# Kernel optimization log

Hardware: AMD Instinct MI355X
Metric: run time of the kernel (lower is better)

The kernel has to match this reference:

```python
import jax, jax.numpy as jnp
import numpy as np

N_NODES = 50000
N_EDGES = 800000
NUM_FEATURES = 128
HIDDEN = 128
EMBED = 64
OUT_DIM = 1


def setup_inputs() -> dict:
    key = jax.random.key(0)
    ks = jax.random.split(key, 12)
    x = jax.random.normal(ks[0], (N_NODES, NUM_FEATURES), dtype=jnp.float32)
    edge_index = jax.random.randint(ks[1], (2, N_EDGES), 0, N_NODES, dtype=jnp.int64)

    def glorot(k, fan_in, fan_out):
        s = jnp.sqrt(6.0 / (fan_in + fan_out)).astype(jnp.float32)
        return jax.random.uniform(k, (fan_in, fan_out), jnp.float32, -s, s)

    return {
        "x": x,
        "edge_index": edge_index,
        "W1": glorot(ks[2], NUM_FEATURES, HIDDEN),
        "b1": jnp.zeros((HIDDEN,), jnp.float32),
        "Wh": glorot(ks[3], HIDDEN, HIDDEN),
        "bh": jnp.zeros((HIDDEN,), jnp.float32),
        "W2": glorot(ks[4], HIDDEN, EMBED),
        "b2": jnp.zeros((EMBED,), jnp.float32),
        "Wout": glorot(ks[5], EMBED, OUT_DIM),
        "bout": jnp.zeros((OUT_DIM,), jnp.float32),
    }


def _gcn_norm(edge_index, num_nodes):
    # Add self-loops, compute symmetric normalization deg^{-1/2} A_hat deg^{-1/2}
    loop = jnp.arange(num_nodes, dtype=edge_index.dtype)
    src = jnp.concatenate([edge_index[0], loop])
    dst = jnp.concatenate([edge_index[1], loop])
    deg = jax.ops.segment_sum(jnp.ones_like(dst, dtype=jnp.float32), dst,
                              num_segments=num_nodes)
    dis = jnp.where(deg > 0, jax.lax.rsqrt(jnp.maximum(deg, 1.0)), 0.0)
    norm = dis[src] * dis[dst]  # [E+N]
    return src, dst, norm


def _gcn_conv(h, W, b, src, dst, norm, num_nodes):
    h = h @ W  # linear transform first (PyG GCNConv)
    msg = h[src] * norm[:, None]  # gather + scale
    return jax.ops.segment_sum(msg, dst, num_segments=num_nodes) + b


def reference(x, edge_index, W1, b1, Wh, bh, W2, b2, Wout, bout):
    n = x.shape[0]
    src, dst, norm = _gcn_norm(edge_index, n)
    h = jax.nn.relu(_gcn_conv(x, W1, b1, src, dst, norm, n))  # dropout p=0 -> identity
    h = jax.nn.relu(_gcn_conv(h, Wh, bh, src, dst, norm, n))
    h = _gcn_conv(h, W2, b2, src, dst, norm, n)
    out = h @ Wout + bout
    return (out, h)
```

## Files before the change

kernel.cpp:

```cpp
#include <hip/hip_runtime.h>
#include <hip/hip_bf16.h>


#define N_NODES 50000
#define N_EDGES 800000
#define NBUCK 196
#define GB 196
#define EPB 4096

typedef __attribute__((ext_vector_type(8))) short short8;
typedef __attribute__((ext_vector_type(8))) unsigned short ushort8v;
typedef __attribute__((ext_vector_type(4))) float f32x4;

static __device__ __forceinline__ unsigned short f2bf(float f) {
    __hip_bfloat16 h = __float2bfloat16(f);
    return *reinterpret_cast<unsigned short*>(&h);
}
static __device__ __forceinline__ float bf2f(unsigned short u) {
    return __uint_as_float(((unsigned)u) << 16);
}


__global__ __launch_bounds__(256) void hist_wprep_kernel(
    const int* __restrict__ dstv, int* __restrict__ H, int nE, int* __restrict__ ticket,
    const float* __restrict__ W1, const float* __restrict__ Wh, const float* __restrict__ W2,
    unsigned short* __restrict__ W1hi, unsigned short* __restrict__ W1lo,
    unsigned short* __restrict__ Whhi, unsigned short* __restrict__ Whlo,
    unsigned short* __restrict__ W2hi, unsigned short* __restrict__ W2lo) {
    int gt = blockIdx.x * 256 + threadIdx.x;
    if (gt == 0) *ticket = 0;
    if (gt < 40960) {
        const float* W;
        unsigned short *Hi, *Lo;
        int nout, lt;
        if (gt < 16384)      { W = W1; Hi = W1hi; Lo = W1lo; nout = 128; lt = gt; }
        else if (gt < 32768) { W = Wh; Hi = Whhi; Lo = Whlo; nout = 128; lt = gt - 16384; }
        else                 { W = W2; Hi = W2hi; Lo = W2lo; nout = 64;  lt = gt - 32768; }
        int col = lt % nout, k = lt / nout;
        float v = W[lt];
        unsigned short hi = f2bf(v);
        unsigned short lo = f2bf(v - bf2f(hi));
        Hi[(size_t)col * 128 + k] = hi;
        Lo[(size_t)col * 128 + k] = lo;
    }

    __shared__ int h[NBUCK];
    for (int i = threadIdx.x; i < NBUCK; i += 256) h[i] = 0;
    __syncthreads();
    int base = blockIdx.x * EPB;
#pragma unroll
    for (int i = 0; i < EPB / 256; ++i) {
        int e = base + i * 256 + threadIdx.x;
        if (e < nE) atomicAdd(&h[dstv[e] >> 8], 1);
    }
    __syncthreads();
    for (int i = threadIdx.x; i < NBUCK; i += 256)
        H[i * GB + blockIdx.x] = h[i];
}

__global__ __launch_bounds__(256) void scan_kernel(int* __restrict__ H,
                                                   int* __restrict__ bsum,
                                                   int* __restrict__ bstart,
                                                   int* __restrict__ rowoff_last,
                                                   int* __restrict__ ticket) {
    __shared__ int s[256];
    __shared__ int lastFlag;
    int t = threadIdx.x;
    int k = blockIdx.x;
    int v = (t < GB) ? H[k * GB + t] : 0;
    s[t] = v;
    __syncthreads();
    for (int off = 1; off < 256; off <<= 1) {
        int u = (t >= off) ? s[t - off] : 0;
        __syncthreads();
        s[t] += u;
        __syncthreads();
    }
    if (t < GB) H[k * GB + t] = s[t] - v;
    if (t == 255) {
        bsum[k] = s[255];
        __threadfence();
        int tk = atomicAdd(ticket, 1);
        lastFlag = (tk == NBUCK - 1);
    }
    __syncthreads();
    if (!lastFlag) return;
    __threadfence();
    int v2 = (t < NBUCK) ? bsum[t] : 0;
    s[t] = v2;
    __syncthreads();
    for (int off = 1; off < 256; off <<= 1) {
        int u = (t >= off) ? s[t - off] : 0;
        __syncthreads();
        s[t] += u;
        __syncthreads();
    }
    if (t < NBUCK) bstart[t] = s[t] - v2;
    if (t == 0) {
        bstart[NBUCK] = N_EDGES;
        *rowoff_last = N_EDGES;
    }
}

__global__ __launch_bounds__(256) void partition_kernel(const int* __restrict__ srcv,
                                                        const int* __restrict__ dstv,
                                                        const int* __restrict__ H,
                                                        const int* __restrict__ bstart,
                                                        unsigned int* __restrict__ P, int nE) {
    __shared__ int cur[NBUCK];
    for (int i = threadIdx.x; i < NBUCK; i += 256)
        cur[i] = bstart[i] + H[i * GB + blockIdx.x];
    __syncthreads();
    int base = blockIdx.x * EPB;
#pragma unroll
    for (int i = 0; i < EPB / 256; ++i) {
        int e = base + i * 256 + threadIdx.x;
        if (e < nE) {
            int d = dstv[e];
            unsigned int pk = (unsigned int)srcv[e] | ((unsigned int)(d & 255) << 16);
            int pos = atomicAdd(&cur[d >> 8], 1);
            P[pos] = pk;
        }
    }
}

__global__ __launch_bounds__(256) void bucket_csr_kernel(const unsigned int* __restrict__ P,
                                                         const int* __restrict__ bstart,
                                                         int* __restrict__ rowoff,
                                                         float* __restrict__ dis,
                                                         unsigned short* __restrict__ csr_src, int n) {
    __shared__ int cnt[256];
    __shared__ int s[256];
    __shared__ int cur[256];
    int t = threadIdx.x;
    int k = blockIdx.x;
    int ebeg = bstart[k], eend = bstart[k + 1];
    cnt[t] = 0;
    __syncthreads();
    for (int e = ebeg + t; e < eend; e += 256)
        atomicAdd(&cnt[(P[e] >> 16) & 255], 1);
    __syncthreads();
    int myc = cnt[t];
    s[t] = myc;
    __syncthreads();
    for (int off = 1; off < 256; off <<= 1) {
        int v = (t >= off) ? s[t - off] : 0;
        __syncthreads();
        s[t] += v;
        __syncthreads();
    }
    int excl = s[t] - myc;
    int node = (k << 8) + t;
    if (node < n) {
        rowoff[node] = ebeg + excl;
        dis[node] = rsqrtf((float)(myc + 1));
    }
    cur[t] = ebeg + excl;
    __syncthreads();
    for (int e = ebeg + t; e < eend; e += 256) {
        unsigned int p = P[e];
        int pos = atomicAdd(&cur[(p >> 16) & 255], 1);
        csr_src[pos] = (unsigned short)(p & 0xFFFFu);
    }
}

template <int NOUT, bool SPLITA>
__global__ __launch_bounds__(256) void gemm_mfma_kernel(
    const float* __restrict__ A,
    const unsigned short* __restrict__ Ahi,
    const unsigned short* __restrict__ Alo,
    const unsigned short* __restrict__ Wthi,
    const unsigned short* __restrict__ Wtlo,
    const float* __restrict__ scale,
    unsigned short* __restrict__ C, int M) {
    constexpr int LDK = 136;
    __shared__ unsigned short sAhi[64 * LDK];
    __shared__ unsigned short sAlo[64 * LDK];

    int tid = threadIdx.x;
    int w = tid >> 6, lane = tid & 63;
    int quad = lane >> 4, m = lane & 15;
    int Rbase = blockIdx.x * 64;
    int Cbase = blockIdx.y * 64;
    int r0 = (w & 1) * 32, c0 = (w >> 1) * 32;

    short8 bh[4][2], bl[4][2];
#pragma unroll
    for (int ks = 0; ks < 4; ++ks)
#pragma unroll
        for (int g = 0; g < 2; ++g) {
            size_t off = (size_t)(Cbase + c0 + g * 16 + m) * 128 + ks * 32 + quad * 8;
            bh[ks][g] = *(const short8*)(Wthi + off);
            bl[ks][g] = *(const short8*)(Wtlo + off);
        }

    if constexpr (SPLITA) {
        for (int i = tid; i < 64 * 16; i += 256) {
            int r = i >> 4, c8 = i & 15;
            int row = Rbase + r;
            short8 hv = {0, 0, 0, 0, 0, 0, 0, 0};
            short8 lv = {0, 0, 0, 0, 0, 0, 0, 0};
            if (row < M) {
                hv = *(const short8*)(Ahi + (size_t)row * 128 + c8 * 8);
                lv = *(const short8*)(Alo + (size_t)row * 128 + c8 * 8);
            }
            *(short8*)(sAhi + r * LDK + c8 * 8) = hv;
            *(short8*)(sAlo + r * LDK + c8 * 8) = lv;
        }
    } else {
        for (int i = tid; i < 64 * 32; i += 256) {
            int r = i >> 5, c4 = i & 31;
            int row = Rbase + r;
            float4 v = make_float4(0.f, 0.f, 0.f, 0.f);
            if (row < M) v = ((const float4*)(A + (size_t)row * 128))[c4];
            ushort4 hi, lo;
            hi.x = f2bf(v.x); lo.x = f2bf(v.x - bf2f(hi.x));
            hi.y = f2bf(v.y); lo.y = f2bf(v.y - bf2f(hi.y));
            hi.z = f2bf(v.z); lo.z = f2bf(v.z - bf2f(hi.z));
            hi.w = f2bf(v.w); lo.w = f2bf(v.w - bf2f(hi.w));
            *(ushort4*)(sAhi + r * LDK + c4 * 4) = hi;
            *(ushort4*)(sAlo + r * LDK + c4 * 4) = lo;
        }
    }
    __syncthreads();

    f32x4 z = {0.f, 0.f, 0.f, 0.f};
    f32x4 acc00 = z, acc01 = z, acc10 = z, acc11 = z;

#pragma unroll
    for (int ks = 0; ks < 4; ++ks) {
        int kof = ks * 32 + quad * 8;
        short8 ah0 = *(const short8*)(sAhi + (r0 + m) * LDK + kof);
        short8 ah1 = *(const short8*)(sAhi + (r0 + 16 + m) * LDK + kof);
        short8 al0 = *(const short8*)(sAlo + (r0 + m) * LDK + kof);
        short8 al1 = *(const short8*)(sAlo + (r0 + 16 + m) * LDK + kof);
        acc00 = __builtin_amdgcn_mfma_f32_16x16x32_bf16(ah0, bh[ks][0], acc00, 0, 0, 0);
        acc01 = __builtin_amdgcn_mfma_f32_16x16x32_bf16(ah0, bh[ks][1], acc01, 0, 0, 0);
        acc10 = __builtin_amdgcn_mfma_f32_16x16x32_bf16(ah1, bh[ks][0], acc10, 0, 0, 0);
        acc11 = __builtin_amdgcn_mfma_f32_16x16x32_bf16(ah1, bh[ks][1], acc11, 0, 0, 0);
        acc00 = __builtin_amdgcn_mfma_f32_16x16x32_bf16(ah0, bl[ks][0], acc00, 0, 0, 0);
        acc01 = __builtin_amdgcn_mfma_f32_16x16x32_bf16(ah0, bl[ks][1], acc01, 0, 0, 0);
        acc10 = __builtin_amdgcn_mfma_f32_16x16x32_bf16(ah1, bl[ks][0], acc10, 0, 0, 0);
        acc11 = __builtin_amdgcn_mfma_f32_16x16x32_bf16(ah1, bl[ks][1], acc11, 0, 0, 0);
        acc00 = __builtin_amdgcn_mfma_f32_16x16x32_bf16(al0, bh[ks][0], acc00, 0, 0, 0);
        acc01 = __builtin_amdgcn_mfma_f32_16x16x32_bf16(al0, bh[ks][1], acc01, 0, 0, 0);
        acc10 = __builtin_amdgcn_mfma_f32_16x16x32_bf16(al1, bh[ks][0], acc10, 0, 0, 0);
        acc11 = __builtin_amdgcn_mfma_f32_16x16x32_bf16(al1, bh[ks][1], acc11, 0, 0, 0);
    }

#pragma unroll
    for (int reg = 0; reg < 4; ++reg) {
        int row0g = Rbase + r0 + quad * 4 + reg;
        if (row0g < M) {
            float sc = scale[row0g];
            C[(size_t)row0g * NOUT + Cbase + c0 + m]      = f2bf(acc00[reg] * sc);
            C[(size_t)row0g * NOUT + Cbase + c0 + 16 + m] = f2bf(acc01[reg] * sc);
        }
        int row1g = row0g + 16;
        if (row1g < M) {
            float sc = scale[row1g];
            C[(size_t)row1g * NOUT + Cbase + c0 + m]      = f2bf(acc10[reg] * sc);
            C[(size_t)row1g * NOUT + Cbase + c0 + 16 + m] = f2bf(acc11[reg] * sc);
        }
    }
}

__global__ __launch_bounds__(256) void aggregate128_kernel(
    const int* __restrict__ rowoff, const unsigned short* __restrict__ csr_src,
    const float* __restrict__ dis, const unsigned short* __restrict__ tp,
    const float* __restrict__ bias,
    unsigned short* __restrict__ outHi, unsigned short* __restrict__ outLo, int n) {
    int wid = (blockIdx.x * 256 + threadIdx.x) >> 6;
    int lane = threadIdx.x & 63;
    int sub = lane >> 4, lc = lane & 15;
    int n0 = wid * 2;
    if (n0 >= n) return;
    int n1 = n0 + 1;
    bool has1 = (n1 < n);

    float a0[8] = {0.f, 0.f, 0.f, 0.f, 0.f, 0.f, 0.f, 0.f};
    float a1[8] = {0.f, 0.f, 0.f, 0.f, 0.f, 0.f, 0.f, 0.f};

#define ROW128(node) (*(const ushort8v*)(tp + (size_t)(node) * 128 + lc * 8))
#define ACC(a, u) { a[0] += bf2f(u[0]); a[1] += bf2f(u[1]); a[2] += bf2f(u[2]); a[3] += bf2f(u[3]); \
                    a[4] += bf2f(u[4]); a[5] += bf2f(u[5]); a[6] += bf2f(u[6]); a[7] += bf2f(u[7]); }

    if (sub == 0) { ushort8v u = ROW128(n0); ACC(a0, u); }
    else if (sub == 1 && has1) { ushort8v u = ROW128(n1); ACC(a1, u); }

    int mid = rowoff[n0 + 1];
    int i0 = rowoff[n0] + sub;
    int i1 = mid + sub;
    int end1 = has1 ? rowoff[n1 + 1] : mid;

    while (i0 + 12 < mid && i1 + 12 < end1) {
        int p0 = csr_src[i0], p1 = csr_src[i0 + 4], p2 = csr_src[i0 + 8], p3 = csr_src[i0 + 12];
        int q0 = csr_src[i1], q1 = csr_src[i1 + 4], q2 = csr_src[i1 + 8], q3 = csr_src[i1 + 12];
        ushort8v u0 = ROW128(p0), u1 = ROW128(p1), u2 = ROW128(p2), u3 = ROW128(p3);
        ushort8v v0 = ROW128(q0), v1 = ROW128(q1), v2 = ROW128(q2), v3 = ROW128(q3);
        ACC(a0, u0); ACC(a0, u1); ACC(a0, u2); ACC(a0, u3);
        ACC(a1, v0); ACC(a1, v1); ACC(a1, v2); ACC(a1, v3);
        i0 += 16; i1 += 16;
    }
    while (i0 + 4 < mid && i1 + 4 < end1) {
        int p0 = csr_src[i0], p1 = csr_src[i0 + 4];
        int q0 = csr_src[i1], q1 = csr_src[i1 + 4];
        ushort8v u0 = ROW128(p0), u1 = ROW128(p1);
        ushort8v v0 = ROW128(q0), v1 = ROW128(q1);
        ACC(a0, u0); ACC(a0, u1);
        ACC(a1, v0); ACC(a1, v1);
        i0 += 8; i1 += 8;
    }
    for (; i0 + 4 < mid; i0 += 8) {
        int p0 = csr_src[i0], p1 = csr_src[i0 + 4];
        ushort8v u0 = ROW128(p0), u1 = ROW128(p1);
        ACC(a0, u0); ACC(a0, u1);
    }
    for (; i0 < mid; i0 += 4) { ushort8v u = ROW128(csr_src[i0]); ACC(a0, u); }
    for (; i1 + 4 < end1; i1 += 8) {
        int q0 = csr_src[i1], q1 = csr_src[i1 + 4];
        ushort8v v0 = ROW128(q0), v1 = ROW128(q1);
        ACC(a1, v0); ACC(a1, v1);
    }
    for (; i1 < end1; i1 += 4) { ushort8v v = ROW128(csr_src[i1]); ACC(a1, v); }
#undef ROW128
#undef ACC

#pragma unroll
    for (int j = 0; j < 8; ++j) {
        a0[j] += __shfl_xor(a0[j], 16);
        a0[j] += __shfl_xor(a0[j], 32);
        a1[j] += __shfl_xor(a1[j], 16);
        a1[j] += __shfl_xor(a1[j], 32);
    }

    float* ap = (sub == 0) ? a0 : a1;
    int node = (sub == 0) ? n0 : n1;
    bool valid = (sub == 0) || (sub == 1 && has1);
    if (valid) {
        float dd = dis[node];
        float4 b0 = ((const float4*)bias)[lc * 2];
        float4 b1v = ((const float4*)bias)[lc * 2 + 1];
        float r[8];
        r[0] = fmaxf(ap[0] * dd + b0.x, 0.f);
        r[1] = fmaxf(ap[1] * dd + b0.y, 0.f);
        r[2] = fmaxf(ap[2] * dd + b0.z, 0.f);
        r[3] = fmaxf(ap[3] * dd + b0.w, 0.f);
        r[4] = fmaxf(ap[4] * dd + b1v.x, 0.f);
        r[5] = fmaxf(ap[5] * dd + b1v.y, 0.f);
        r[6] = fmaxf(ap[6] * dd + b1v.z, 0.f);
        r[7] = fmaxf(ap[7] * dd + b1v.w, 0.f);
        ushort8v hi, lo;
#pragma unroll
        for (int j = 0; j < 8; ++j) {
            hi[j] = f2bf(r[j]);
            lo[j] = f2bf(r[j] - bf2f(hi[j]));
        }
        *(ushort8v*)(outHi + (size_t)node * 128 + lc * 8) = hi;
        *(ushort8v*)(outLo + (size_t)node * 128 + lc * 8) = lo;
    }
}

__global__ __launch_bounds__(256) void aggregate64_head_kernel(
    const int* __restrict__ rowoff, const unsigned short* __restrict__ csr_src,
    const float* __restrict__ dis, const unsigned short* __restrict__ tp,
    const float* __restrict__ bias, const float* __restrict__ Wout,
    const float* __restrict__ bout, float* __restrict__ hout,
    float* __restrict__ out, int n) {
    int wid = (blockIdx.x * 256 + threadIdx.x) >> 6;
    int lane = threadIdx.x & 63;
    int sub = lane >> 4, lc = lane & 15;
    int n0 = wid * 2;
    if (n0 >= n) return;
    int n1 = n0 + 1;
    bool has1 = (n1 < n);

    float a0[4] = {0.f, 0.f, 0.f, 0.f};
    float a1[4] = {0.f, 0.f, 0.f, 0.f};

#define ROW64(node) (*((const ushort4*)(tp + (size_t)(node) * 64 + lc * 4)))
#define ACC2(a, u) { a[0] += bf2f(u.x); a[1] += bf2f(u.y); a[2] += bf2f(u.z); a[3] += bf2f(u.w); }

    if (sub == 0) { ushort4 u = ROW64(n0); ACC2(a0, u); }
    else if (sub == 1 && has1) { ushort4 u = ROW64(n1); ACC2(a1, u); }

    int mid = rowoff[n0 + 1];
    int i0 = rowoff[n0] + sub;
    int i1 = mid + sub;
    int end1 = has1 ? rowoff[n1 + 1] : mid;

    while (i0 + 12 < mid && i1 + 12 < end1) {
        int p0 = csr_src[i0], p1 = csr_src[i0 + 4], p2 = csr_src[i0 + 8], p3 = csr_src[i0 + 12];
        int q0 = csr_src[i1], q1 = csr_src[i1 + 4], q2 = csr_src[i1 + 8], q3 = csr_src[i1 + 12];
        ushort4 u0 = ROW64(p0), u1 = ROW64(p1), u2 = ROW64(p2), u3 = ROW64(p3);
        ushort4 v0 = ROW64(q0), v1 = ROW64(q1), v2 = ROW64(q2), v3 = ROW64(q3);
        ACC2(a0, u0); ACC2(a0, u1); ACC2(a0, u2); ACC2(a0, u3);
        ACC2(a1, v0); ACC2(a1, v1); ACC2(a1, v2); ACC2(a1, v3);
        i0 += 16; i1 += 16;
    }
    while (i0 + 4 < mid && i1 + 4 < end1) {
        int p0 = csr_src[i0], p1 = csr_src[i0 + 4];
        int q0 = csr_src[i1], q1 = csr_src[i1 + 4];
        ushort4 u0 = ROW64(p0), u1 = ROW64(p1);
        ushort4 v0 = ROW64(q0), v1 = ROW64(q1);
        ACC2(a0, u0); ACC2(a0, u1);
        ACC2(a1, v0); ACC2(a1, v1);
        i0 += 8; i1 += 8;
    }
    for (; i0 < mid; i0 += 4) { ushort4 u = ROW64(csr_src[i0]); ACC2(a0, u); }
    for (; i1 < end1; i1 += 4) { ushort4 v = ROW64(csr_src[i1]); ACC2(a1, v); }
#undef ROW64
#undef ACC2

#pragma unroll
    for (int j = 0; j < 4; ++j) {
        a0[j] += __shfl_xor(a0[j], 16);
        a0[j] += __shfl_xor(a0[j], 32);
        a1[j] += __shfl_xor(a1[j], 16);
        a1[j] += __shfl_xor(a1[j], 32);
    }

    float* ap = (sub == 0) ? a0 : a1;
    int node = (sub == 0) ? n0 : n1;
    bool valid = (sub == 0) || (sub == 1 && has1);
    float4 hv = make_float4(0.f, 0.f, 0.f, 0.f);
    if (valid) {
        float dd = dis[node];
        float4 b = ((const float4*)bias)[lc];
        hv.x = ap[0] * dd + b.x;
        hv.y = ap[1] * dd + b.y;
        hv.z = ap[2] * dd + b.z;
        hv.w = ap[3] * dd + b.w;
        ((float4*)(hout + (size_t)node * 64))[lc] = hv;
    }
    float4 wv = ((const float4*)Wout)[lc];
    float p = valid ? (hv.x * wv.x + hv.y * wv.y + hv.z * wv.z + hv.w * wv.w) : 0.f;
#pragma unroll
    for (int off = 8; off > 0; off >>= 1) p += __shfl_xor(p, off);
    if (lc == 0 && valid) out[node] = p + bout[0];
}

extern "C" void kernel_launch(void* const* d_in, const int* in_sizes, int n_in,
                              void* d_out, int out_size, void* d_ws, size_t ws_size,
                              hipStream_t stream) {
    const float* x    = (const float*)d_in[0];
    const int*   ei   = (const int*)d_in[1];
    const float* W1   = (const float*)d_in[2];
    const float* b1   = (const float*)d_in[3];
    const float* Wh   = (const float*)d_in[4];
    const float* bh   = (const float*)d_in[5];
    const float* W2   = (const float*)d_in[6];
    const float* b2   = (const float*)d_in[7];
    const float* Wout = (const float*)d_in[8];
    const float* bout = (const float*)d_in[9];

    const int N = N_NODES;
    const int E = N_EDGES;
    const int* srcv = ei;
    const int* dstv = ei + E;

    float* out  = (float*)d_out;
    float* hout = (float*)d_out + N;

    char* ws = (char*)d_ws;
    auto alloc = [&](size_t bytes) -> char* {
        char* p = ws;
        ws += (bytes + 255) & ~(size_t)255;
        return p;
    };
    int*   H       = (int*)alloc(sizeof(int) * NBUCK * GB);
    int*   bsum    = (int*)alloc(sizeof(int) * NBUCK);
    int*   bstart  = (int*)alloc(sizeof(int) * (NBUCK + 1));
    int*   ticket  = (int*)alloc(sizeof(int) * 4);
    int*   rowoff  = (int*)alloc(sizeof(int) * (N + 1));
    unsigned int* P = (unsigned int*)alloc(sizeof(unsigned int) * E);
    unsigned short* csr_src = (unsigned short*)alloc(sizeof(unsigned short) * (E + 2));
    float* dis     = (float*)alloc(sizeof(float) * N);
    unsigned short* W1thi = (unsigned short*)alloc(sizeof(unsigned short) * 128 * 128);
    unsigned short* W1tlo = (unsigned short*)alloc(sizeof(unsigned short) * 128 * 128);
    unsigned short* Whthi = (unsigned short*)alloc(sizeof(unsigned short) * 128 * 128);
    unsigned short* Whtlo = (unsigned short*)alloc(sizeof(unsigned short) * 128 * 128);
    unsigned short* W2thi = (unsigned short*)alloc(sizeof(unsigned short) * 64 * 128);
    unsigned short* W2tlo = (unsigned short*)alloc(sizeof(unsigned short) * 64 * 128);
    unsigned short* bufT  = (unsigned short*)alloc(sizeof(unsigned short) * (size_t)N * 128);
    unsigned short* bufHi = (unsigned short*)alloc(sizeof(unsigned short) * (size_t)N * 128);
    unsigned short* bufLo = (unsigned short*)alloc(sizeof(unsigned short) * (size_t)N * 128);

    hist_wprep_kernel<<<GB, 256, 0, stream>>>(dstv, H, E, ticket,
                                              W1, Wh, W2, W1thi, W1tlo, Whthi, Whtlo, W2thi, W2tlo);
    scan_kernel<<<NBUCK, 256, 0, stream>>>(H, bsum, bstart, rowoff + N, ticket);
    partition_kernel<<<GB, 256, 0, stream>>>(srcv, dstv, H, bstart, P, E);
    bucket_csr_kernel<<<NBUCK, 256, 0, stream>>>(P, bstart, rowoff, dis, csr_src, N);

    const int aggBlocks = ((N + 1) / 2 * 64 + 255) / 256;
    const int gemmRows = (N + 63) / 64;

    gemm_mfma_kernel<128, false><<<dim3(gemmRows, 2), 256, 0, stream>>>(
        x, nullptr, nullptr, W1thi, W1tlo, dis, bufT, N);
    aggregate128_kernel<<<aggBlocks, 256, 0, stream>>>(
        rowoff, csr_src, dis, bufT, b1, bufHi, bufLo, N);

    gemm_mfma_kernel<128, true><<<dim3(gemmRows, 2), 256, 0, stream>>>(
        nullptr, bufHi, bufLo, Whthi, Whtlo, dis, bufT, N);
    aggregate128_kernel<<<aggBlocks, 256, 0, stream>>>(
        rowoff, csr_src, dis, bufT, bh, bufHi, bufLo, N);

    gemm_mfma_kernel<64, true><<<dim3(gemmRows, 1), 256, 0, stream>>>(
        nullptr, bufHi, bufLo, W2thi, W2tlo, dis, bufT, N);
    aggregate64_head_kernel<<<aggBlocks, 256, 0, stream>>>(
        rowoff, csr_src, dis, bufT, b2, Wout, bout, hout, out, N);
}
```

Baseline: 277.9 us.

## Assign one 16-lane group per node in aggregation, dropping cross-lane reductions

```diff
diff --git a/kernel.cpp b/kernel.cpp
--- a/kernel.cpp
+++ b/kernel.cpp
@@ -19,7 +19,6 @@
 static __device__ __forceinline__ float bf2f(unsigned short u) {
     return __uint_as_float(((unsigned)u) << 16);
 }
-
 
 __global__ __launch_bounds__(256) void hist_wprep_kernel(
     const int* __restrict__ dstv, int* __restrict__ H, int nE, int* __restrict__ ticket,
@@ -30,9 +29,7 @@
     int gt = blockIdx.x * 256 + threadIdx.x;
     if (gt == 0) *ticket = 0;
     if (gt < 40960) {
-        const float* W;
-        unsigned short *Hi, *Lo;
-        int nout, lt;
+        const float* W; unsigned short *Hi, *Lo; int nout, lt;
         if (gt < 16384)      { W = W1; Hi = W1hi; Lo = W1lo; nout = 128; lt = gt; }
         else if (gt < 32768) { W = Wh; Hi = Whhi; Lo = Whlo; nout = 128; lt = gt - 16384; }
         else                 { W = W2; Hi = W2hi; Lo = W2lo; nout = 64;  lt = gt - 32768; }
@@ -65,8 +62,7 @@
                                                    int* __restrict__ ticket) {
     __shared__ int s[256];
     __shared__ int lastFlag;
-    int t = threadIdx.x;
-    int k = blockIdx.x;
+    int t = threadIdx.x, k = blockIdx.x;
     int v = (t < GB) ? H[k * GB + t] : 0;
     s[t] = v;
     __syncthreads();
@@ -96,10 +92,7 @@
         __syncthreads();
     }
     if (t < NBUCK) bstart[t] = s[t] - v2;
-    if (t == 0) {
-        bstart[NBUCK] = N_EDGES;
-        *rowoff_last = N_EDGES;
-    }
+    if (t == 0) { bstart[NBUCK] = N_EDGES; *rowoff_last = N_EDGES; }
 }
 
 __global__ __launch_bounds__(256) void partition_kernel(const int* __restrict__ srcv,
@@ -132,8 +125,7 @@
     __shared__ int cnt[256];
     __shared__ int s[256];
     __shared__ int cur[256];
-    int t = threadIdx.x;
-    int k = blockIdx.x;
+    int t = threadIdx.x, k = blockIdx.x;
     int ebeg = bstart[k], eend = bstart[k + 1];
     cnt[t] = 0;
     __syncthreads();
@@ -167,12 +159,9 @@
 template <int NOUT, bool SPLITA>
 __global__ __launch_bounds__(256) void gemm_mfma_kernel(
     const float* __restrict__ A,
-    const unsigned short* __restrict__ Ahi,
-    const unsigned short* __restrict__ Alo,
-    const unsigned short* __restrict__ Wthi,
-    const unsigned short* __restrict__ Wtlo,
-    const float* __restrict__ scale,
-    unsigned short* __restrict__ C, int M) {
+    const unsigned short* __restrict__ Ahi, const unsigned short* __restrict__ Alo,
+    const unsigned short* __restrict__ Wthi, const unsigned short* __restrict__ Wtlo,
+    const float* __restrict__ scale, unsigned short* __restrict__ C, int M) {
     constexpr int LDK = 136;
     __shared__ unsigned short sAhi[64 * LDK];
     __shared__ unsigned short sAlo[64 * LDK];
@@ -180,8 +169,7 @@
     int tid = threadIdx.x;
     int w = tid >> 6, lane = tid & 63;
     int quad = lane >> 4, m = lane & 15;
-    int Rbase = blockIdx.x * 64;
-    int Cbase = blockIdx.y * 64;
+    int Rbase = blockIdx.x * 64, Cbase = blockIdx.y * 64;
     int r0 = (w & 1) * 32, c0 = (w >> 1) * 32;
 
     short8 bh[4][2], bl[4][2];
@@ -198,8 +186,7 @@
         for (int i = tid; i < 64 * 16; i += 256) {
             int r = i >> 4, c8 = i & 15;
             int row = Rbase + r;
-            short8 hv = {0, 0, 0, 0, 0, 0, 0, 0};
-            short8 lv = {0, 0, 0, 0, 0, 0, 0, 0};
+            short8 hv = {0,0,0,0,0,0,0,0}, lv = {0,0,0,0,0,0,0,0};
             if (row < M) {
                 hv = *(const short8*)(Ahi + (size_t)row * 128 + c8 * 8);
                 lv = *(const short8*)(Alo + (size_t)row * 128 + c8 * 8);
@@ -270,95 +257,63 @@
     const float* __restrict__ dis, const unsigned short* __restrict__ tp,
     const float* __restrict__ bias,
     unsigned short* __restrict__ outHi, unsigned short* __restrict__ outLo, int n) {
-    int wid = (blockIdx.x * 256 + threadIdx.x) >> 6;
-    int lane = threadIdx.x & 63;
-    int sub = lane >> 4, lc = lane & 15;
-    int n0 = wid * 2;
-    if (n0 >= n) return;
-    int n1 = n0 + 1;
-    bool has1 = (n1 < n);
-
-    float a0[8] = {0.f, 0.f, 0.f, 0.f, 0.f, 0.f, 0.f, 0.f};
-    float a1[8] = {0.f, 0.f, 0.f, 0.f, 0.f, 0.f, 0.f, 0.f};
-
-#define ROW128(node) (*(const ushort8v*)(tp + (size_t)(node) * 128 + lc * 8))
-#define ACC(a, u) { a[0] += bf2f(u[0]); a[1] += bf2f(u[1]); a[2] += bf2f(u[2]); a[3] += bf2f(u[3]); \
-                    a[4] += bf2f(u[4]); a[5] += bf2f(u[5]); a[6] += bf2f(u[6]); a[7] += bf2f(u[7]); }
-
-    if (sub == 0) { ushort8v u = ROW128(n0); ACC(a0, u); }
-    else if (sub == 1 && has1) { ushort8v u = ROW128(n1); ACC(a1, u); }
-
-    int mid = rowoff[n0 + 1];
-    int i0 = rowoff[n0] + sub;
-    int i1 = mid + sub;
-    int end1 = has1 ? rowoff[n1 + 1] : mid;
-
-    while (i0 + 12 < mid && i1 + 12 < end1) {
-        int p0 = csr_src[i0], p1 = csr_src[i0 + 4], p2 = csr_src[i0 + 8], p3 = csr_src[i0 + 12];
-        int q0 = csr_src[i1], q1 = csr_src[i1 + 4], q2 = csr_src[i1 + 8], q3 = csr_src[i1 + 12];
+    int gt = blockIdx.x * 256 + threadIdx.x;
+    int node = gt >> 4;
+    if (node >= n) return;
+    int lc = gt & 15;
+
+    float a[8] = {0.f,0.f,0.f,0.f,0.f,0.f,0.f,0.f};
+
+#define ROW128(nd) (*(const ushort8v*)(tp + (size_t)(nd) * 128 + lc * 8))
+#define ACC(u) { a[0] += bf2f(u[0]); a[1] += bf2f(u[1]); a[2] += bf2f(u[2]); a[3] += bf2f(u[3]); \
+                 a[4] += bf2f(u[4]); a[5] += bf2f(u[5]); a[6] += bf2f(u[6]); a[7] += bf2f(u[7]); }
+
+    { ushort8v u = ROW128(node); ACC(u); }
+
+    int i = rowoff[node], end = rowoff[node + 1];
+    for (; i + 8 <= end; i += 8) {
+        int p0 = csr_src[i],     p1 = csr_src[i + 1], p2 = csr_src[i + 2], p3 = csr_src[i + 3];
+        int p4 = csr_src[i + 4], p5 = csr_src[i + 5], p6 = csr_src[i + 6], p7 = csr_src[i + 7];
         ushort8v u0 = ROW128(p0), u1 = ROW128(p1), u2 = ROW128(p2), u3 = ROW128(p3);
-        ushort8v v0 = ROW128(q0), v1 = ROW128(q1), v2 = ROW128(q2), v3 = ROW128(q3);
-        ACC(a0, u0); ACC(a0, u1); ACC(a0, u2); ACC(a0, u3);
-        ACC(a1, v0); ACC(a1, v1); ACC(a1, v2); ACC(a1, v3);
-        i0 += 16; i1 += 16;
-    }
-    while (i0 + 4 < mid && i1 + 4 < end1) {
-        int p0 = csr_src[i0], p1 = csr_src[i0 + 4];
-        int q0 = csr_src[i1], q1 = csr_src[i1 + 4];
+        ushort8v u4 = ROW128(p4), u5 = ROW128(p5), u6 = ROW128(p6), u7 = ROW128(p7);
+        ACC(u0); ACC(u1); ACC(u2); ACC(u3); ACC(u4); ACC(u5); ACC(u6); ACC(u7);
+    }
+    if (i + 4 <= end) {
+        int p0 = csr_src[i], p1 = csr_src[i + 1], p2 = csr_src[i + 2], p3 = csr_src[i + 3];
+        ushort8v u0 = ROW128(p0), u1 = ROW128(p1), u2 = ROW128(p2), u3 = ROW128(p3);
+        ACC(u0); ACC(u1); ACC(u2); ACC(u3);
+        i += 4;
+    }
+    if (i + 2 <= end) {
+        int p0 = csr_src[i], p1 = csr_src[i + 1];
         ushort8v u0 = ROW128(p0), u1 = ROW128(p1);
-        ushort8v v0 = ROW128(q0), v1 = ROW128(q1);
-        ACC(a0, u0); ACC(a0, u1);
-        ACC(a1, v0); ACC(a1, v1);
-        i0 += 8; i1 += 8;
-    }
-    for (; i0 + 4 < mid; i0 += 8) {
-        int p0 = csr_src[i0], p1 = csr_src[i0 + 4];
-        ushort8v u0 = ROW128(p0), u1 = ROW128(p1);
-        ACC(a0, u0); ACC(a0, u1);
-    }
-    for (; i0 < mid; i0 += 4) { ushort8v u = ROW128(csr_src[i0]); ACC(a0, u); }
-    for (; i1 + 4 < end1; i1 += 8) {
-        int q0 = csr_src[i1], q1 = csr_src[i1 + 4];
-        ushort8v v0 = ROW128(q0), v1 = ROW128(q1);
-        ACC(a1, v0); ACC(a1, v1);
-    }
-    for (; i1 < end1; i1 += 4) { ushort8v v = ROW128(csr_src[i1]); ACC(a1, v); }
+        ACC(u0); ACC(u1);
+        i += 2;
+    }
+    if (i < end) { ushort8v u = ROW128(csr_src[i]); ACC(u); }
 #undef ROW128
 #undef ACC
 
+    float dd = dis[node];
+    float4 b0 = ((const float4*)bias)[lc * 2];
+    float4 b1 = ((const float4*)bias)[lc * 2 + 1];
+    float r[8];
+    r[0] = fmaxf(a[0] * dd + b0.x, 0.f);
+    r[1] = fmaxf(a[1] * dd + b0.y, 0.f);
+    r[2] = fmaxf(a[2] * dd + b0.z, 0.f);
+    r[3] = fmaxf(a[3] * dd + b0.w, 0.f);
+    r[4] = fmaxf(a[4] * dd + b1.x, 0.f);
+    r[5] = fmaxf(a[5] * dd + b1.y, 0.f);
+    r[6] = fmaxf(a[6] * dd + b1.z, 0.f);
+    r[7] = fmaxf(a[7] * dd + b1.w, 0.f);
+    ushort8v hi, lo;
 #pragma unroll
     for (int j = 0; j < 8; ++j) {
-        a0[j] += __shfl_xor(a0[j], 16);
-        a0[j] += __shfl_xor(a0[j], 32);
-        a1[j] += __shfl_xor(a1[j], 16);
-        a1[j] += __shfl_xor(a1[j], 32);
-    }
-
-    float* ap = (sub == 0) ? a0 : a1;
-    int node = (sub == 0) ? n0 : n1;
-    bool valid = (sub == 0) || (sub == 1 && has1);
-    if (valid) {
-        float dd = dis[node];
-        float4 b0 = ((const float4*)bias)[lc * 2];
-        float4 b1v = ((const float4*)bias)[lc * 2 + 1];
-        float r[8];
-        r[0] = fmaxf(ap[0] * dd + b0.x, 0.f);
-        r[1] = fmaxf(ap[1] * dd + b0.y, 0.f);
-        r[2] = fmaxf(ap[2] * dd + b0.z, 0.f);
-        r[3] = fmaxf(ap[3] * dd + b0.w, 0.f);
-        r[4] = fmaxf(ap[4] * dd + b1v.x, 0.f);
-        r[5] = fmaxf(ap[5] * dd + b1v.y, 0.f);
-        r[6] = fmaxf(ap[6] * dd + b1v.z, 0.f);
-        r[7] = fmaxf(ap[7] * dd + b1v.w, 0.f);
-        ushort8v hi, lo;
-#pragma unroll
-        for (int j = 0; j < 8; ++j) {
-            hi[j] = f2bf(r[j]);
-            lo[j] = f2bf(r[j] - bf2f(hi[j]));
-        }
-        *(ushort8v*)(outHi + (size_t)node * 128 + lc * 8) = hi;
-        *(ushort8v*)(outLo + (size_t)node * 128 + lc * 8) = lo;
-    }
+        hi[j] = f2bf(r[j]);
+        lo[j] = f2bf(r[j] - bf2f(hi[j]));
+    }
+    *(ushort8v*)(outHi + (size_t)node * 128 + lc * 8) = hi;
+    *(ushort8v*)(outLo + (size_t)node * 128 + lc * 8) = lo;
 }
 
 __global__ __launch_bounds__(256) void aggregate64_head_kernel(
@@ -367,77 +322,56 @@
     const float* __restrict__ bias, const float* __restrict__ Wout,
     const float* __restrict__ bout, float* __restrict__ hout,
     float* __restrict__ out, int n) {
-    int wid = (blockIdx.x * 256 + threadIdx.x) >> 6;
-    int lane = threadIdx.x & 63;
-    int sub = lane >> 4, lc = lane & 15;
-    int n0 = wid * 2;
-    if (n0 >= n) return;
-    int n1 = n0 + 1;
-    bool has1 = (n1 < n);
-
-    float a0[4] = {0.f, 0.f, 0.f, 0.f};
-    float a1[4] = {0.f, 0.f, 0.f, 0.f};
-
-#define ROW64(node) (*((const ushort4*)(tp + (size_t)(node) * 64 + lc * 4)))
-#define ACC2(a, u) { a[0] += bf2f(u.x); a[1] += bf2f(u.y); a[2] += bf2f(u.z); a[3] += bf2f(u.w); }
-
-    if (sub == 0) { ushort4 u = ROW64(n0); ACC2(a0, u); }
-    else if (sub == 1 && has1) { ushort4 u = ROW64(n1); ACC2(a1, u); }
-
-    int mid = rowoff[n0 + 1];
-    int i0 = rowoff[n0] + sub;
-    int i1 = mid + sub;
-    int end1 = has1 ? rowoff[n1 + 1] : mid;
-
-    while (i0 + 12 < mid && i1 + 12 < end1) {
-        int p0 = csr_src[i0], p1 = csr_src[i0 + 4], p2 = csr_src[i0 + 8], p3 = csr_src[i0 + 12];
-        int q0 = csr_src[i1], q1 = csr_src[i1 + 4], q2 = csr_src[i1 + 8], q3 = csr_src[i1 + 12];
+    int gt = blockIdx.x * 256 + threadIdx.x;
+    int node = gt >> 4;
+    if (node >= n) return;
+    int lc = gt & 15;
+
+    float a[4] = {0.f,0.f,0.f,0.f};
+
+#define ROW64(nd) (*((const ushort4*)(tp + (size_t)(nd) * 64 + lc * 4)))
+#define ACC2(u) { a[0] += bf2f(u.x); a[1] += bf2f(u.y); a[2] += bf2f(u.z); a[3] += bf2f(u.w); }
+
+    { ushort4 u = ROW64(node); ACC2(u); }
+
+    int i = rowoff[node], end = rowoff[node + 1];
+    for (; i + 8 <= end; i += 8) {
+        int p0 = csr_src[i],     p1 = csr_src[i + 1], p2 = csr_src[i + 2], p3 = csr_src[i + 3];
+        int p4 = csr_src[i + 4], p5 = csr_src[i + 5], p6 = csr_src[i + 6], p7 = csr_src[i + 7];
         ushort4 u0 = ROW64(p0), u1 = ROW64(p1), u2 = ROW64(p2), u3 = ROW64(p3);
-        ushort4 v0 = ROW64(q0), v1 = ROW64(q1), v2 = ROW64(q2), v3 = ROW64(q3);
-        ACC2(a0, u0); ACC2(a0, u1); ACC2(a0, u2); ACC2(a0, u3);
-        ACC2(a1, v0); ACC2(a1, v1); ACC2(a1, v2); ACC2(a1, v3);
-        i0 += 16; i1 += 16;
-    }
-    while (i0 + 4 < mid && i1 + 4 < end1) {
-        int p0 = csr_src[i0], p1 = csr_src[i0 + 4];
-        int q0 = csr_src[i1], q1 = csr_src[i1 + 4];
+        ushort4 u4 = ROW64(p4), u5 = ROW64(p5), u6 = ROW64(p6), u7 = ROW64(p7);
+        ACC2(u0); ACC2(u1); ACC2(u2); ACC2(u3); ACC2(u4); ACC2(u5); ACC2(u6); ACC2(u7);
+    }
+    if (i + 4 <= end) {
+        int p0 = csr_src[i], p1 = csr_src[i + 1], p2 = csr_src[i + 2], p3 = csr_src[i + 3];
+        ushort4 u0 = ROW64(p0), u1 = ROW64(p1), u2 = ROW64(p2), u3 = ROW64(p3);
+        ACC2(u0); ACC2(u1); ACC2(u2); ACC2(u3);
+        i += 4;
+    }
+    if (i + 2 <= end) {
+        int p0 = csr_src[i], p1 = csr_src[i + 1];
         ushort4 u0 = ROW64(p0), u1 = ROW64(p1);
-        ushort4 v0 = ROW64(q0), v1 = ROW64(q1);
-        ACC2(a0, u0); ACC2(a0, u1);
-        ACC2(a1, v0); ACC2(a1, v1);
-        i0 += 8; i1 += 8;
-    }
-    for (; i0 < mid; i0 += 4) { ushort4 u = ROW64(csr_src[i0]); ACC2(a0, u); }
-    for (; i1 < end1; i1 += 4) { ushort4 v = ROW64(csr_src[i1]); ACC2(a1, v); }
+        ACC2(u0); ACC2(u1);
+        i += 2;
+    }
+    if (i < end) { ushort4 u = ROW64(csr_src[i]); ACC2(u); }
 #undef ROW64
 #undef ACC2
 
-#pragma unroll
-    for (int j = 0; j < 4; ++j) {
-        a0[j] += __shfl_xor(a0[j], 16);
-        a0[j] += __shfl_xor(a0[j], 32);
-        a1[j] += __shfl_xor(a1[j], 16);
-        a1[j] += __shfl_xor(a1[j], 32);
-    }
-
-    float* ap = (sub == 0) ? a0 : a1;
-    int node = (sub == 0) ? n0 : n1;
-    bool valid = (sub == 0) || (sub == 1 && has1);
-    float4 hv = make_float4(0.f, 0.f, 0.f, 0.f);
-    if (valid) {
-        float dd = dis[node];
-        float4 b = ((const float4*)bias)[lc];
-        hv.x = ap[0] * dd + b.x;
-        hv.y = ap[1] * dd + b.y;
-        hv.z = ap[2] * dd + b.z;
-        hv.w = ap[3] * dd + b.w;
-        ((float4*)(hout + (size_t)node * 64))[lc] = hv;
-    }
+    float dd = dis[node];
+    float4 b = ((const float4*)bias)[lc];
+    float4 hv;
+    hv.x = a[0] * dd + b.x;
+    hv.y = a[1] * dd + b.y;
+    hv.z = a[2] * dd + b.z;
+    hv.w = a[3] * dd + b.w;
+    ((float4*)(hout + (size_t)node * 64))[lc] = hv;
+
     float4 wv = ((const float4*)Wout)[lc];
-    float p = valid ? (hv.x * wv.x + hv.y * wv.y + hv.z * wv.z + hv.w * wv.w) : 0.f;
+    float p = hv.x * wv.x + hv.y * wv.y + hv.z * wv.z + hv.w * wv.w;
 #pragma unroll
     for (int off = 8; off > 0; off >>= 1) p += __shfl_xor(p, off);
-    if (lc == 0 && valid) out[node] = p + bout[0];
+    if (lc == 0) out[node] = p + bout[0];
 }
 
 extern "C" void kernel_launch(void* const* d_in, const int* in_sizes, int n_in,
@@ -474,7 +408,7 @@
     int*   ticket  = (int*)alloc(sizeof(int) * 4);
     int*   rowoff  = (int*)alloc(sizeof(int) * (N + 1));
     unsigned int* P = (unsigned int*)alloc(sizeof(unsigned int) * E);
-    unsigned short* csr_src = (unsigned short*)alloc(sizeof(unsigned short) * (E + 2));
+    unsigned short* csr_src = (unsigned short*)alloc(sizeof(unsigned short) * (E + 8));
     float* dis     = (float*)alloc(sizeof(float) * N);
     unsigned short* W1thi = (unsigned short*)alloc(sizeof(unsigned short) * 128 * 128);
     unsigned short* W1tlo = (unsigned short*)alloc(sizeof(unsigned short) * 128 * 128);
@@ -492,7 +426,7 @@
     partition_kernel<<<GB, 256, 0, stream>>>(srcv, dstv, H, bstart, P, E);
     bucket_csr_kernel<<<NBUCK, 256, 0, stream>>>(P, bstart, rowoff, dis, csr_src, N);
 
-    const int aggBlocks = ((N + 1) / 2 * 64 + 255) / 256;
+    const int aggBlocks = (N * 16 + 255) / 256;
     const int gemmRows = (N + 63) / 64;
 
     gemm_mfma_kernel<128, false><<<dim3(gemmRows, 2), 256, 0, stream>>>(
```

Measured after the change: 258.9 us. -6.8%, faster.
